# Performance work log

Hardware: AMD Instinct MI355X
Metric: run time of the kernel (lower is better)

The kernel has to match this reference:

```python
import jax, jax.numpy as jnp
import numpy as np

K, N, NE, NI, MA, IN, B = 8, 512, 256, 256, 3, 128, 1024
H, UNFOLDS = 0.04, 6
DT = H / UNFOLDS
STATE = NE * MA + NI * MA + NE + NI + N  # 2560


def inv_softplus(x):
    return float(np.log(np.expm1(x)))


def piecewise_sigmoid(x, S_a=0.9, S_c=0.0):
    a = S_a / 2.0
    c = S_c
    k = 0.5 / (1.0 - 2.0 * a)  # = 5.0 for S_a=0.9
    x1, x2, x3, x4 = c + a - 1.0, c - a, c + a, c + 1.0 - a
    quad_rise = k * (x - x1) * (x - x1)
    linear = x - c + 0.5
    quad_cap = 1.0 - k * (x - x4) * (x - x4)
    out = jnp.where(x < x1, 0.0, quad_rise)
    out = jnp.where(x >= x2, linear, out)
    out = jnp.where(x > x3, quad_cap, out)
    out = jnp.where(x > x4, 1.0, out)
    return out


def setup_inputs():
    key = jax.random.key(0)
    ks = jax.random.split(key, 6)
    m = (jax.random.uniform(ks[0], (K, N, N)) > 0.5).astype(jnp.float32)  # sparsity masks
    W_raw = jax.random.normal(ks[1], (K, N, N)) * np.float32(np.sqrt(2.0 / N)) * m
    W_in = jax.random.normal(ks[2], (K, N, IN)) * 0.1
    lo, hi = inv_softplus(0.25), inv_softplus(10.0)
    taus = jnp.asarray([lo + (hi - lo) * ai / (MA - 1) for ai in range(MA)], dtype=jnp.float32)
    log_tau_a = jnp.tile(taus[None, None, :], (K, NE, 1))
    return {
        "inputs": jax.random.normal(ks[3], (B, IN), dtype=jnp.float32),
        "state": jax.random.uniform(ks[4], (K, B, STATE), dtype=jnp.float32),
        "W_raw": W_raw,
        "sparsity_masks": m,
        "W_in": W_in,
        "a_0": jnp.full((K, N), 0.35, jnp.float32),
        "log_tau_d": jnp.full((K, N), inv_softplus(0.1), jnp.float32),
        "log_tau_a_E": log_tau_a,
        "log_c_E": jnp.full((K, NE, MA), -3.0, jnp.float32),
        "c_0_E": jnp.zeros((K, NE, MA), jnp.float32),
        "log_tau_a_I": log_tau_a,
        "log_c_I": jnp.full((K, NI, MA), -3.0, jnp.float32),
        "c_0_I": jnp.zeros((K, NI, MA), jnp.float32),
        "log_tau_b_rec_E": jnp.full((K, NE), inv_softplus(1.0), jnp.float32),
        "log_tau_b_rel_E": jnp.full((K, NE), inv_softplus(0.25), jnp.float32),
        "log_tau_b_rec_I": jnp.full((K, NI), inv_softplus(1.0), jnp.float32),
        "log_tau_b_rel_I": jnp.full((K, NI), inv_softplus(0.25), jnp.float32),
        "readout_ids": jnp.zeros((K,), dtype=jnp.int32),  # 0=synaptic,1=rate,2=dendritic
    }


def _forward(inputs, state, W_raw, sparsity_masks, W_in, a_0, log_tau_d,
             log_tau_a_E, log_c_E, c_0_E, log_tau_a_I, log_c_I, c_0_I,
             log_tau_b_rec_E, log_tau_b_rel_E, log_tau_b_rec_I, log_tau_b_rel_I,
             readout_ids):
    sp = jax.nn.softplus
    # unpack flat state (K,B,STATE)
    i0 = NE * MA; i1 = i0 + NI * MA; i2 = i1 + NE; i3 = i2 + NI
    aE = state[:, :, :i0].reshape(K, B, NE, MA)
    aI = state[:, :, i0:i1].reshape(K, B, NI, MA)
    bE = state[:, :, i1:i2]          # (K,B,NE)
    bI = state[:, :, i2:i3]          # (K,B,NI)
    x = state[:, :, i3:]             # (K,B,N)
    # Dale-constrained effective recurrent weights
    W_pos = sp(W_raw)
    W_eff = jnp.concatenate([W_pos[:, :, :NE], -W_pos[:, :, NE:]], axis=2) * sparsity_masks
    # time-constant gains
    gx = DT / sp(log_tau_d)[:, None]                    # (K,1,N)
    gaE = DT / sp(log_tau_a_E)[:, None]                 # (K,1,NE,MA)
    gaI = DT / sp(log_tau_a_I)[:, None]
    cE = sp(log_c_E)[:, None]                           # (K,1,NE,MA)
    cI = sp(log_c_I)[:, None]
    grecE = (DT / sp(log_tau_b_rec_E))[:, None]         # (K,1,NE)
    grelE = (DT / sp(log_tau_b_rel_E))[:, None]
    grecI = (DT / sp(log_tau_b_rec_I))[:, None]
    grelI = (DT / sp(log_tau_b_rel_I))[:, None]
    in_cur = jnp.einsum('kni,bi->kbn', W_in, inputs)    # constant across unfolds

    def rate_syn(aE, aI, bE, bI, x):
        thr = a_0[:, None] + jnp.concatenate(
            [jnp.sum(aE + c_0_E[:, None], axis=-1),
             jnp.sum(aI + c_0_I[:, None], axis=-1)], axis=-1)
        r = piecewise_sigmoid(x - thr)                  # (K,B,N)
        s = r * jnp.concatenate([bE, bI], axis=-1)      # depression-scaled output
        return r, s

    def step(carry, _):
        aE, aI, bE, bI, x = carry
        r, s = rate_syn(aE, aI, bE, bI, x)
        rE, rI = r[..., :NE], r[..., NE:]
        syn = jnp.einsum('knm,kbm->kbn', W_eff, s) + in_cur
        x = (x + gx * syn) / (1.0 + gx)                 # semi-implicit Euler
        aE = (aE + gaE * cE * rE[..., None]) / (1.0 + gaE)
        aI = (aI + gaI * cI * rI[..., None]) / (1.0 + gaI)
        bE = (bE + grecE) / (1.0 + grecE + grelE * rE)
        bI = (bI + grecI) / (1.0 + grecI + grelI * rI)
        return (aE, aI, bE, bI, x), None

    (aE, aI, bE, bI, x), _ = jax.lax.scan(step, (aE, aI, bE, bI, x), None, length=UNFOLDS)
    r, s = rate_syn(aE, aI, bE, bI, x)
    rid = readout_ids[:, None, None]
    out = jnp.where(rid == 0, s, jnp.where(rid == 1, r, x))
    new_state = jnp.concatenate(
        [aE.reshape(K, B, -1), aI.reshape(K, B, -1), bE, bI, x], axis=-1)
    return out, new_state


def reference(inputs, state, W_raw, sparsity_masks, W_in, a_0, log_tau_d,
              log_tau_a_E, log_c_E, c_0_E, log_tau_a_I, log_c_I, c_0_I,
              log_tau_b_rec_E, log_tau_b_rel_E, log_tau_b_rec_I, log_tau_b_rel_I,
              readout_ids):
    return _forward(inputs, state, W_raw, sparsity_masks, W_in, a_0, log_tau_d,
                    log_tau_a_E, log_c_E, c_0_E, log_tau_a_I, log_c_I, c_0_I,
                    log_tau_b_rec_E, log_tau_b_rel_E, log_tau_b_rec_I, log_tau_b_rel_I,
                    readout_ids)
```

## Files before the change

### kernel.cpp

```cpp
#include <hip/hip_runtime.h>
#include <stdint.h>

#define K_ 8
#define N_ 512
#define NE_ 256
#define MA_ 3
#define IN_ 128
#define B_ 1024
#define STATE_ 2560
#define UNFOLDS_ 6
#define DT_ (0.04f / 6.0f)

typedef __attribute__((ext_vector_type(8))) short short8;
typedef __attribute__((ext_vector_type(4))) float floatx4;

__device__ __forceinline__ float b2f(uint16_t u) {
    union { uint32_t i; float f; } v; v.i = ((uint32_t)u) << 16; return v.f;
}
__device__ __forceinline__ uint16_t f2b(float f) {
    union { float f; uint32_t i; } v; v.f = f;
    uint32_t i = v.i;
    uint32_t r = i + 0x7FFFu + ((i >> 16) & 1u);
    return (uint16_t)(r >> 16);
}
__device__ __forceinline__ uint32_t pack2(uint16_t lo, uint16_t hi) {
    return (uint32_t)lo | ((uint32_t)hi << 16);
}
__device__ __forceinline__ float loadf(const void* p, size_t i, int f32) {
    return f32 ? ((const float*)p)[i] : b2f(((const uint16_t*)p)[i]);
}
__device__ __forceinline__ float ntloadf(const void* p, size_t i, int f32) {
    return f32 ? __builtin_nontemporal_load((const float*)p + i)
               : b2f(__builtin_nontemporal_load((const uint16_t*)p + i));
}
__device__ __forceinline__ float spf(float x) {
    return (x > 20.f) ? x : log1pf(expf(x));
}
__device__ __forceinline__ float psig(float x) {
    float t1 = x + 0.55f;
    float q1 = 5.f * t1 * t1;
    float t2 = x - 0.55f;
    float q2 = 1.f - 5.f * t2 * t2;
    float out = (x < -0.55f) ? 0.f : q1;
    out = (x >= -0.45f) ? (x + 0.5f) : out;
    out = (x > 0.45f) ? q2 : out;
    out = (x > 0.55f) ? 1.f : out;
    return out;
}

__global__ void srnn_detect_kernel(const uint16_t* canary, int* flag) {
    __shared__ int cnt;
    if (threadIdx.x == 0) cnt = 0;
    __syncthreads();
    int bad = 0;
    for (int i = threadIdx.x; i < 4096; i += 256) {
        uint16_t u = canary[i];
        int e = (u >> 7) & 0xFF;
        if (e >= 0xC0) bad++;
    }
    atomicAdd(&cnt, bad);
    __syncthreads();
    if (threadIdx.x == 0) flag[0] = (cnt >= 16) ? 1 : 0;
}

__global__ void srnn_params_kernel(
    const void* a0, const void* ltd,
    const void* ltaE, const void* lcE, const void* c0E,
    const void* ltaI, const void* lcI, const void* c0I,
    const void* lbrecE, const void* lbrelE,
    const void* lbrecI, const void* lbrelI,
    const int* flag, float* P)
{
    const int f = flag[0];
    int idx = blockIdx.x * 256 + threadIdx.x;
    if (idx >= K_ * N_) return;
    int n = idx & (N_ - 1);
    int k = idx >> 9;
    float gx = DT_ / spf(loadf(ltd, idx, f));
    float thr0 = loadf(a0, idx, f);

    const void *lta, *lc, *c0, *lbrec, *lbrel;
    int nn;
    if (n < NE_) { nn = n;        lta = ltaE; lc = lcE; c0 = c0E; lbrec = lbrecE; lbrel = lbrelE; }
    else         { nn = n - NE_;  lta = ltaI; lc = lcI; c0 = c0I; lbrec = lbrecI; lbrel = lbrelI; }
    int base3 = (k * NE_ + nn) * MA_;
    int base1 = k * NE_ + nn;

    float amul[3], ainv[3];
    #pragma unroll
    for (int j = 0; j < 3; ++j) {
        float ga = DT_ / spf(loadf(lta, base3 + j, f));
        float c  = spf(loadf(lc, base3 + j, f));
        amul[j] = ga * c;
        ainv[j] = 1.f / (1.f + ga);
        thr0 += loadf(c0, base3 + j, f);
    }
    float grec = DT_ / spf(loadf(lbrec, base1, f));
    float grel = DT_ / spf(loadf(lbrel, base1, f));

    const int KN = K_ * N_;
    P[0*KN + idx] = gx;
    P[1*KN + idx] = 1.f / (1.f + gx);
    P[2*KN + idx] = thr0;
    P[3*KN + idx] = grec;
    P[4*KN + idx] = grel;
    P[5*KN + idx] = amul[0]; P[6*KN + idx] = amul[1]; P[7*KN + idx] = amul[2];
    P[8*KN + idx] = ainv[0]; P[9*KN + idx] = ainv[1]; P[10*KN + idx] = ainv[2];
}

__global__ __launch_bounds__(256) void srnn_wsw_kernel(
    const void* __restrict__ Wraw, const void* __restrict__ mask,
    const int* __restrict__ flag, uint16_t* __restrict__ Wsw)
{
    __shared__ float tile[16 * 516];
    const int f = flag[0];
    const int nt = blockIdx.x, k = blockIdx.y, t = threadIdx.x;
    const size_t base = (size_t)k * N_ * N_ + (size_t)nt * 16 * N_;
    #pragma unroll
    for (int i = 0; i < 32; ++i) {
        int idx = i * 256 + t;
        int row = idx >> 9, m = idx & 511;
        size_t gi = base + (size_t)row * N_ + m;
        float w = spf(ntloadf(Wraw, gi, f)) * ntloadf(mask, gi, f);
        if (m >= NE_) w = -w;
        tile[row * 516 + m] = w;
    }
    __syncthreads();
    uint16_t* outb = Wsw + ((size_t)k * 32 + nt) * (16 * 64 * 8);
    #pragma unroll
    for (int i = 0; i < 4; ++i) {
        int id = i * 256 + t;
        int ks = id >> 6, L = id & 63;
        int row = L & 15, quad = L >> 4;
        const float* src = &tile[row * 516 + ks * 32 + quad * 8];
        uint4 v;
        v.x = pack2(f2b(src[0]), f2b(src[1]));
        v.y = pack2(f2b(src[2]), f2b(src[3]));
        v.z = pack2(f2b(src[4]), f2b(src[5]));
        v.w = pack2(f2b(src[6]), f2b(src[7]));
        *(uint4*)(outb + (size_t)id * 8) = v;
    }
}

__global__ __launch_bounds__(256) void srnn_winsw_kernel(
    const void* __restrict__ Win, const int* __restrict__ flag,
    uint16_t* __restrict__ Winsw)
{
    __shared__ float tile[16 * 132];
    const int f = flag[0];
    const int nt = blockIdx.x, k = blockIdx.y, t = threadIdx.x;
    const size_t base = (size_t)k * N_ * IN_ + (size_t)nt * 16 * IN_;
    #pragma unroll
    for (int i = 0; i < 8; ++i) {
        int idx = i * 256 + t;
        int row = idx >> 7, c = idx & 127;
        tile[row * 132 + c] = ntloadf(Win, base + (size_t)row * IN_ + c, f);
    }
    __syncthreads();
    uint16_t* outb = Winsw + ((size_t)k * 32 + nt) * (4 * 64 * 8);
    {
        int id = t;
        int ks = id >> 6, L = id & 63;
        int row = L & 15, quad = L >> 4;
        const float* src = &tile[row * 132 + ks * 32 + quad * 8];
        uint4 v;
        v.x = pack2(f2b(src[0]), f2b(src[1]));
        v.y = pack2(f2b(src[2]), f2b(src[3]));
        v.z = pack2(f2b(src[4]), f2b(src[5]));
        v.w = pack2(f2b(src[6]), f2b(src[7]));
        *(uint4*)(outb + (size_t)id * 8) = v;
    }
}

__global__ __launch_bounds__(512, 1)
void srnn_main_kernel(const void* __restrict__ state,
                      const void* __restrict__ inputs,
                      const uint16_t* __restrict__ Wsw,
                      const uint16_t* __restrict__ Winsw,
                      const float* __restrict__ P,
                      const int* __restrict__ readout,
                      const int* __restrict__ flag,
                      void* __restrict__ out)
{
    __shared__ __align__(16) uint16_t sT[16 * 520];
    __shared__ __align__(16) float synT[16 * 516];

    const int f = flag[0];
    const int t = threadIdx.x;
    const int k = blockIdx.x & 7;
    const int b0 = (blockIdx.x >> 3) * 16;
    const int n = t;
    const int lane = t & 63, w = t >> 6;
    const int bq = lane & 15, quad = lane >> 4;

    const int KN = K_ * N_;
    const int pi = k * N_ + n;
    const float gx = P[0*KN+pi], ivgx = P[1*KN+pi], thr0 = P[2*KN+pi];
    const float grec = P[3*KN+pi], grel = P[4*KN+pi];
    const float amul0 = P[5*KN+pi], amul1 = P[6*KN+pi], amul2 = P[7*KN+pi];
    const float ainv0 = P[8*KN+pi], ainv1 = P[9*KN+pi], ainv2 = P[10*KN+pi];

    #pragma unroll
    for (int q = 0; q < 4; ++q) {
        int idx = q * 512 + t;
        int bb = idx >> 7, i = idx & 127;
        sT[bb * 520 + i] = f2b(ntloadf(inputs, (size_t)(b0 + bb) * IN_ + i, f));
    }

    float a0v[16], a1v[16], a2v[16], bv[16], xv[16], ic[16];
    #pragma unroll
    for (int bb = 0; bb < 16; ++bb) {
        size_t sb = ((size_t)k * B_ + b0 + bb) * STATE_;
        a0v[bb] = ntloadf(state, sb + 3 * n + 0, f);
        a1v[bb] = ntloadf(state, sb + 3 * n + 1, f);
        a2v[bb] = ntloadf(state, sb + 3 * n + 2, f);
        bv[bb]  = ntloadf(state, sb + 1536 + n, f);
        xv[bb]  = ntloadf(state, sb + 2048 + n, f);
    }
    __syncthreads();

    const uint16_t* bpe = sT + bq * 520 + quad * 8;

    {
        const uint16_t* api = Winsw + ((size_t)(k * 32 + 4 * w) * 4) * 512 + (size_t)lane * 8;
        floatx4 d0 = {0.f,0.f,0.f,0.f}, d1 = d0, d2 = d0, d3 = d0;
        #pragma unroll
        for (int ks = 0; ks < 4; ++ks) {
            short8 bf = *(const short8*)(bpe + ks * 32);
            short8 a0f = *(const short8*)(api + (0 * 4 + ks) * 512);
            short8 a1f = *(const short8*)(api + (1 * 4 + ks) * 512);
            short8 a2f = *(const short8*)(api + (2 * 4 + ks) * 512);
            short8 a3f = *(const short8*)(api + (3 * 4 + ks) * 512);
            d0 = __builtin_amdgcn_mfma_f32_16x16x32_bf16(a0f, bf, d0, 0, 0, 0);
            d1 = __builtin_amdgcn_mfma_f32_16x16x32_bf16(a1f, bf, d1, 0, 0, 0);
            d2 = __builtin_amdgcn_mfma_f32_16x16x32_bf16(a2f, bf, d2, 0, 0, 0);
            d3 = __builtin_amdgcn_mfma_f32_16x16x32_bf16(a3f, bf, d3, 0, 0, 0);
        }
        const int nb = w * 64 + quad * 4;
        *(floatx4*)(&synT[bq * 516 + nb +  0]) = d0;
        *(floatx4*)(&synT[bq * 516 + nb + 16]) = d1;
        *(floatx4*)(&synT[bq * 516 + nb + 32]) = d2;
        *(floatx4*)(&synT[bq * 516 + nb + 48]) = d3;
    }
    __syncthreads();
    #pragma unroll
    for (int bb = 0; bb < 16; ++bb) ic[bb] = synT[bb * 516 + n];
    __syncthreads();

    const uint16_t* ape = Wsw + (size_t)k * 32 * 8192 + (size_t)(4 * w) * 8192 + (size_t)lane * 8;

    for (int step = 0; step < UNFOLDS_; ++step) {
        #pragma unroll
        for (int bb = 0; bb < 16; ++bb) {
            float thr = thr0 + a0v[bb] + a1v[bb] + a2v[bb];
            float r = psig(xv[bb] - thr);
            float s = r * bv[bb];
            a0v[bb] = fmaf(amul0, r, a0v[bb]) * ainv0;
            a1v[bb] = fmaf(amul1, r, a1v[bb]) * ainv1;
            a2v[bb] = fmaf(amul2, r, a2v[bb]) * ainv2;
            bv[bb] = (bv[bb] + grec) / (1.f + grec + grel * r);
            sT[bb * 520 + n] = f2b(s);
        }
        __syncthreads();

        floatx4 c0 = {0.f, 0.f, 0.f, 0.f}, c1 = c0, c2 = c0, c3 = c0;
        #pragma unroll 4
        for (int ks = 0; ks < 16; ++ks) {
            short8 bf = *(const short8*)(bpe + ks * 32);
            short8 af0 = *(const short8*)(ape + ks * 512);
            short8 af1 = *(const short8*)(ape + 8192 + ks * 512);
            short8 af2 = *(const short8*)(ape + 16384 + ks * 512);
            short8 af3 = *(const short8*)(ape + 24576 + ks * 512);
            c0 = __builtin_amdgcn_mfma_f32_16x16x32_bf16(af0, bf, c0, 0, 0, 0);
            c1 = __builtin_amdgcn_mfma_f32_16x16x32_bf16(af1, bf, c1, 0, 0, 0);
            c2 = __builtin_amdgcn_mfma_f32_16x16x32_bf16(af2, bf, c2, 0, 0, 0);
            c3 = __builtin_amdgcn_mfma_f32_16x16x32_bf16(af3, bf, c3, 0, 0, 0);
        }
        {
            const int nb = w * 64 + quad * 4;
            *(floatx4*)(&synT[bq * 516 + nb +  0]) = c0;
            *(floatx4*)(&synT[bq * 516 + nb + 16]) = c1;
            *(floatx4*)(&synT[bq * 516 + nb + 32]) = c2;
            *(floatx4*)(&synT[bq * 516 + nb + 48]) = c3;
        }
        __syncthreads();

        #pragma unroll
        for (int bb = 0; bb < 16; ++bb) {
            float syn = synT[bb * 516 + n] + ic[bb];
            xv[bb] = fmaf(gx, syn, xv[bb]) * ivgx;
        }
    }

    const int rid = readout[k];
    if (f) {
        float* outp = (float*)out;
        float* nst = outp + (size_t)K_ * B_ * N_;
        #pragma unroll
        for (int bb = 0; bb < 16; ++bb) {
            float thr = thr0 + a0v[bb] + a1v[bb] + a2v[bb];
            float r = psig(xv[bb] - thr);
            float s = r * bv[bb];
            float o = (rid == 0) ? s : ((rid == 1) ? r : xv[bb]);
            size_t ob = (size_t)k * B_ + b0 + bb;
            __builtin_nontemporal_store(o, outp + ob * N_ + n);
            float* st = nst + ob * STATE_;
            __builtin_nontemporal_store(a0v[bb], st + 3 * n + 0);
            __builtin_nontemporal_store(a1v[bb], st + 3 * n + 1);
            __builtin_nontemporal_store(a2v[bb], st + 3 * n + 2);
            __builtin_nontemporal_store(bv[bb], st + 1536 + n);
            __builtin_nontemporal_store(xv[bb], st + 2048 + n);
        }
    } else {
        uint16_t* outp = (uint16_t*)out;
        uint16_t* nst = outp + (size_t)K_ * B_ * N_;
        #pragma unroll
        for (int bb = 0; bb < 16; ++bb) {
            float thr = thr0 + a0v[bb] + a1v[bb] + a2v[bb];
            float r = psig(xv[bb] - thr);
            float s = r * bv[bb];
            float o = (rid == 0) ? s : ((rid == 1) ? r : xv[bb]);
            size_t ob = (size_t)k * B_ + b0 + bb;
            __builtin_nontemporal_store(f2b(o), outp + ob * N_ + n);
            uint16_t* st = nst + ob * STATE_;
            __builtin_nontemporal_store(f2b(a0v[bb]), st + 3 * n + 0);
            __builtin_nontemporal_store(f2b(a1v[bb]), st + 3 * n + 1);
            __builtin_nontemporal_store(f2b(a2v[bb]), st + 3 * n + 2);
            __builtin_nontemporal_store(f2b(bv[bb]), st + 1536 + n);
            __builtin_nontemporal_store(f2b(xv[bb]), st + 2048 + n);
        }
    }
}

extern "C" void kernel_launch(void* const* d_in, const int* in_sizes, int n_in,
                              void* d_out, int out_size, void* d_ws, size_t ws_size,
                              hipStream_t stream) {
    const void* inputs = d_in[0];
    const void* state  = d_in[1];
    const void* Wraw   = d_in[2];
    const void* mask   = d_in[3];
    const void* Win    = d_in[4];
    const void* a0     = d_in[5];
    const void* ltd    = d_in[6];
    const void* ltaE   = d_in[7];
    const void* lcE    = d_in[8];
    const void* c0E    = d_in[9];
    const void* ltaI   = d_in[10];
    const void* lcI    = d_in[11];
    const void* c0I    = d_in[12];
    const void* lbrecE = d_in[13];
    const void* lbrelE = d_in[14];
    const void* lbrecI = d_in[15];
    const void* lbrelI = d_in[16];
    const int* readout = (const int*)d_in[17];

    char* ws = (char*)d_ws;
    int* flag       = (int*)ws;
    float* P        = (float*)(ws + 256);
    uint16_t* Wsw   = (uint16_t*)(ws + 256 + 180224);
    uint16_t* Winsw = (uint16_t*)(ws + 256 + 180224 + 4194304);

    srnn_detect_kernel<<<dim3(1), dim3(256), 0, stream>>>((const uint16_t*)Wraw, flag);
    srnn_params_kernel<<<dim3(16), dim3(256), 0, stream>>>(
        a0, ltd, ltaE, lcE, c0E, ltaI, lcI, c0I, lbrecE, lbrelE, lbrecI, lbrelI, flag, P);
    srnn_wsw_kernel<<<dim3(32, 8), dim3(256), 0, stream>>>(Wraw, mask, flag, Wsw);
    srnn_winsw_kernel<<<dim3(32, 8), dim3(256), 0, stream>>>(Win, flag, Winsw);
    srnn_main_kernel<<<dim3(512), dim3(512), 0, stream>>>(
        state, inputs, Wsw, Winsw, P, readout, flag, d_out);
}
```

Measured before the change: 343.7 us.

## Process 32 batch rows per block, reusing weight fragments across two batch tiles

The main kernel now runs 1024 threads per block covering two 16-row batch sub-tiles, so each loaded W fragment feeds two MFMAs and global weight traffic per batch row is halved. The input projection is folded into every step's MFMA accumulation instead of being precomputed once and held in registers. The x update moves to the start of the next step, and the final x update moves into the epilogue. Per-neuron parameters are staged in shared memory, and the b-update divide is replaced by a fast reciprocal using a precomputed 1+grec. This trades fewer blocks (256), larger shared-memory use and redundant input-projection MFMAs for better weight reuse.

After: 392.5 us. 14.2% more time.

```diff
diff --git a/kernel.cpp b/kernel.cpp
--- a/kernel.cpp
+++ b/kernel.cpp
@@ -106,6 +106,7 @@
     P[4*KN + idx] = grel;
     P[5*KN + idx] = amul[0]; P[6*KN + idx] = amul[1]; P[7*KN + idx] = amul[2];
     P[8*KN + idx] = ainv[0]; P[9*KN + idx] = ainv[1]; P[10*KN + idx] = ainv[2];
+    P[11*KN + idx] = 1.f + grec;
 }
 
 __global__ __launch_bounds__(256) void srnn_wsw_kernel(
@@ -172,7 +173,7 @@
     }
 }
 
-__global__ __launch_bounds__(512, 1)
+__global__ __launch_bounds__(1024, 4)
 void srnn_main_kernel(const void* __restrict__ state,
                       const void* __restrict__ inputs,
                       const uint16_t* __restrict__ Wsw,
@@ -182,35 +183,40 @@
                       const int* __restrict__ flag,
                       void* __restrict__ out)
 {
-    __shared__ __align__(16) uint16_t sT[16 * 520];
-    __shared__ __align__(16) float synT[16 * 516];
+    __shared__ __align__(16) uint16_t sT[2][16 * 520];
+    __shared__ __align__(16) float synT[2][16 * 516];
+    __shared__ __align__(16) uint16_t U[2][16 * 136];
+    __shared__ float Pl[12 * 512];
 
     const int f = flag[0];
     const int t = threadIdx.x;
     const int k = blockIdx.x & 7;
-    const int b0 = (blockIdx.x >> 3) * 16;
-    const int n = t;
+    const int b0 = (blockIdx.x >> 3) * 32;
+    const int sub = t >> 9;
+    const int n = t & 511;
     const int lane = t & 63, w = t >> 6;
     const int bq = lane & 15, quad = lane >> 4;
 
-    const int KN = K_ * N_;
-    const int pi = k * N_ + n;
-    const float gx = P[0*KN+pi], ivgx = P[1*KN+pi], thr0 = P[2*KN+pi];
-    const float grec = P[3*KN+pi], grel = P[4*KN+pi];
-    const float amul0 = P[5*KN+pi], amul1 = P[6*KN+pi], amul2 = P[7*KN+pi];
-    const float ainv0 = P[8*KN+pi], ainv1 = P[9*KN+pi], ainv2 = P[10*KN+pi];
-
+    {
+        const int KN = K_ * N_;
+        #pragma unroll
+        for (int q = 0; q < 6; ++q) {
+            int idx = q * 1024 + t;
+            Pl[idx] = P[(idx >> 9) * KN + k * N_ + (idx & 511)];
+        }
+    }
     #pragma unroll
     for (int q = 0; q < 4; ++q) {
-        int idx = q * 512 + t;
-        int bb = idx >> 7, i = idx & 127;
-        sT[bb * 520 + i] = f2b(ntloadf(inputs, (size_t)(b0 + bb) * IN_ + i, f));
-    }
-
-    float a0v[16], a1v[16], a2v[16], bv[16], xv[16], ic[16];
+        int idx = q * 1024 + t;
+        int ss = idx >> 11, rem = idx & 2047;
+        int bb = rem >> 7, ii = rem & 127;
+        U[ss][bb * 136 + ii] =
+            f2b(ntloadf(inputs, (size_t)(b0 + ss * 16 + bb) * IN_ + ii, f));
+    }
+    float a0v[16], a1v[16], a2v[16], bv[16], xv[16];
     #pragma unroll
     for (int bb = 0; bb < 16; ++bb) {
-        size_t sb = ((size_t)k * B_ + b0 + bb) * STATE_;
+        size_t sb = ((size_t)k * B_ + b0 + sub * 16 + bb) * STATE_;
         a0v[bb] = ntloadf(state, sb + 3 * n + 0, f);
         a1v[bb] = ntloadf(state, sb + 3 * n + 1, f);
         a2v[bb] = ntloadf(state, sb + 3 * n + 2, f);
@@ -219,115 +225,114 @@
     }
     __syncthreads();
 
-    const uint16_t* bpe = sT + bq * 520 + quad * 8;
-
-    {
-        const uint16_t* api = Winsw + ((size_t)(k * 32 + 4 * w) * 4) * 512 + (size_t)lane * 8;
-        floatx4 d0 = {0.f,0.f,0.f,0.f}, d1 = d0, d2 = d0, d3 = d0;
-        #pragma unroll
-        for (int ks = 0; ks < 4; ++ks) {
-            short8 bf = *(const short8*)(bpe + ks * 32);
-            short8 a0f = *(const short8*)(api + (0 * 4 + ks) * 512);
-            short8 a1f = *(const short8*)(api + (1 * 4 + ks) * 512);
-            short8 a2f = *(const short8*)(api + (2 * 4 + ks) * 512);
-            short8 a3f = *(const short8*)(api + (3 * 4 + ks) * 512);
-            d0 = __builtin_amdgcn_mfma_f32_16x16x32_bf16(a0f, bf, d0, 0, 0, 0);
-            d1 = __builtin_amdgcn_mfma_f32_16x16x32_bf16(a1f, bf, d1, 0, 0, 0);
-            d2 = __builtin_amdgcn_mfma_f32_16x16x32_bf16(a2f, bf, d2, 0, 0, 0);
-            d3 = __builtin_amdgcn_mfma_f32_16x16x32_bf16(a3f, bf, d3, 0, 0, 0);
-        }
-        const int nb = w * 64 + quad * 4;
-        *(floatx4*)(&synT[bq * 516 + nb +  0]) = d0;
-        *(floatx4*)(&synT[bq * 516 + nb + 16]) = d1;
-        *(floatx4*)(&synT[bq * 516 + nb + 32]) = d2;
-        *(floatx4*)(&synT[bq * 516 + nb + 48]) = d3;
-    }
-    __syncthreads();
-    #pragma unroll
-    for (int bb = 0; bb < 16; ++bb) ic[bb] = synT[bb * 516 + n];
-    __syncthreads();
-
-    const uint16_t* ape = Wsw + (size_t)k * 32 * 8192 + (size_t)(4 * w) * 8192 + (size_t)lane * 8;
+    const uint16_t* bpe0 = sT[0] + bq * 520 + quad * 8;
+    const uint16_t* bpe1 = sT[1] + bq * 520 + quad * 8;
+    const uint16_t* upe0 = U[0] + bq * 136 + quad * 8;
+    const uint16_t* upe1 = U[1] + bq * 136 + quad * 8;
+    const uint16_t* ape  = Wsw + (size_t)k * 262144 + (size_t)(2 * w) * 8192
+                               + (size_t)lane * 8;
+    const uint16_t* apie = Winsw + (size_t)(k * 32 + 2 * w) * 2048
+                                 + (size_t)lane * 8;
 
     for (int step = 0; step < UNFOLDS_; ++step) {
-        #pragma unroll
-        for (int bb = 0; bb < 16; ++bb) {
-            float thr = thr0 + a0v[bb] + a1v[bb] + a2v[bb];
-            float r = psig(xv[bb] - thr);
-            float s = r * bv[bb];
-            a0v[bb] = fmaf(amul0, r, a0v[bb]) * ainv0;
-            a1v[bb] = fmaf(amul1, r, a1v[bb]) * ainv1;
-            a2v[bb] = fmaf(amul2, r, a2v[bb]) * ainv2;
-            bv[bb] = (bv[bb] + grec) / (1.f + grec + grel * r);
-            sT[bb * 520 + n] = f2b(s);
+        {
+            const float gx = Pl[0*512+n], ivgx = Pl[1*512+n];
+            if (step) {
+                #pragma unroll
+                for (int bb = 0; bb < 16; ++bb)
+                    xv[bb] = fmaf(gx, synT[sub][bb * 516 + n], xv[bb]) * ivgx;
+            }
+            const float thr0 = Pl[2*512+n], grec = Pl[3*512+n], grel = Pl[4*512+n];
+            const float am0 = Pl[5*512+n], am1 = Pl[6*512+n], am2 = Pl[7*512+n];
+            const float ai0 = Pl[8*512+n], ai1 = Pl[9*512+n], ai2 = Pl[10*512+n];
+            const float ogr = Pl[11*512+n];
+            #pragma unroll
+            for (int bb = 0; bb < 16; ++bb) {
+                float thr = thr0 + a0v[bb] + a1v[bb] + a2v[bb];
+                float r = psig(xv[bb] - thr);
+                float s = r * bv[bb];
+                a0v[bb] = fmaf(am0, r, a0v[bb]) * ai0;
+                a1v[bb] = fmaf(am1, r, a1v[bb]) * ai1;
+                a2v[bb] = fmaf(am2, r, a2v[bb]) * ai2;
+                bv[bb] = (bv[bb] + grec) *
+                         __builtin_amdgcn_rcpf(fmaf(grel, r, ogr));
+                sT[sub][bb * 520 + n] = f2b(s);
+            }
         }
         __syncthreads();
 
-        floatx4 c0 = {0.f, 0.f, 0.f, 0.f}, c1 = c0, c2 = c0, c3 = c0;
-        #pragma unroll 4
-        for (int ks = 0; ks < 16; ++ks) {
-            short8 bf = *(const short8*)(bpe + ks * 32);
-            short8 af0 = *(const short8*)(ape + ks * 512);
-            short8 af1 = *(const short8*)(ape + 8192 + ks * 512);
-            short8 af2 = *(const short8*)(ape + 16384 + ks * 512);
-            short8 af3 = *(const short8*)(ape + 24576 + ks * 512);
-            c0 = __builtin_amdgcn_mfma_f32_16x16x32_bf16(af0, bf, c0, 0, 0, 0);
-            c1 = __builtin_amdgcn_mfma_f32_16x16x32_bf16(af1, bf, c1, 0, 0, 0);
-            c2 = __builtin_amdgcn_mfma_f32_16x16x32_bf16(af2, bf, c2, 0, 0, 0);
-            c3 = __builtin_amdgcn_mfma_f32_16x16x32_bf16(af3, bf, c3, 0, 0, 0);
-        }
         {
-            const int nb = w * 64 + quad * 4;
-            *(floatx4*)(&synT[bq * 516 + nb +  0]) = c0;
-            *(floatx4*)(&synT[bq * 516 + nb + 16]) = c1;
-            *(floatx4*)(&synT[bq * 516 + nb + 32]) = c2;
-            *(floatx4*)(&synT[bq * 516 + nb + 48]) = c3;
+            floatx4 c00 = {0.f,0.f,0.f,0.f}, c01 = c00, c10 = c00, c11 = c00;
+            #pragma unroll 2
+            for (int ks = 0; ks < 16; ++ks) {
+                short8 bf0 = *(const short8*)(bpe0 + ks * 32);
+                short8 bf1 = *(const short8*)(bpe1 + ks * 32);
+                short8 af0 = *(const short8*)(ape + ks * 512);
+                short8 af1 = *(const short8*)(ape + 8192 + ks * 512);
+                c00 = __builtin_amdgcn_mfma_f32_16x16x32_bf16(af0, bf0, c00, 0, 0, 0);
+                c01 = __builtin_amdgcn_mfma_f32_16x16x32_bf16(af0, bf1, c01, 0, 0, 0);
+                c10 = __builtin_amdgcn_mfma_f32_16x16x32_bf16(af1, bf0, c10, 0, 0, 0);
+                c11 = __builtin_amdgcn_mfma_f32_16x16x32_bf16(af1, bf1, c11, 0, 0, 0);
+            }
+            #pragma unroll
+            for (int e = 0; e < 4; ++e) {
+                short8 bu0 = *(const short8*)(upe0 + e * 32);
+                short8 bu1 = *(const short8*)(upe1 + e * 32);
+                short8 aw0 = *(const short8*)(apie + e * 512);
+                short8 aw1 = *(const short8*)(apie + 2048 + e * 512);
+                c00 = __builtin_amdgcn_mfma_f32_16x16x32_bf16(aw0, bu0, c00, 0, 0, 0);
+                c01 = __builtin_amdgcn_mfma_f32_16x16x32_bf16(aw0, bu1, c01, 0, 0, 0);
+                c10 = __builtin_amdgcn_mfma_f32_16x16x32_bf16(aw1, bu0, c10, 0, 0, 0);
+                c11 = __builtin_amdgcn_mfma_f32_16x16x32_bf16(aw1, bu1, c11, 0, 0, 0);
+            }
+            const int nb = w * 32 + quad * 4;
+            *(floatx4*)(&synT[0][bq * 516 + nb +  0]) = c00;
+            *(floatx4*)(&synT[0][bq * 516 + nb + 16]) = c10;
+            *(floatx4*)(&synT[1][bq * 516 + nb +  0]) = c01;
+            *(floatx4*)(&synT[1][bq * 516 + nb + 16]) = c11;
         }
         __syncthreads();
-
-        #pragma unroll
-        for (int bb = 0; bb < 16; ++bb) {
-            float syn = synT[bb * 516 + n] + ic[bb];
-            xv[bb] = fmaf(gx, syn, xv[bb]) * ivgx;
-        }
     }
 
     const int rid = readout[k];
+    const float gx = Pl[0*512+n], ivgx = Pl[1*512+n], thr0 = Pl[2*512+n];
     if (f) {
         float* outp = (float*)out;
         float* nst = outp + (size_t)K_ * B_ * N_;
         #pragma unroll
         for (int bb = 0; bb < 16; ++bb) {
+            float x = fmaf(gx, synT[sub][bb * 516 + n], xv[bb]) * ivgx;
             float thr = thr0 + a0v[bb] + a1v[bb] + a2v[bb];
-            float r = psig(xv[bb] - thr);
+            float r = psig(x - thr);
             float s = r * bv[bb];
-            float o = (rid == 0) ? s : ((rid == 1) ? r : xv[bb]);
-            size_t ob = (size_t)k * B_ + b0 + bb;
+            float o = (rid == 0) ? s : ((rid == 1) ? r : x);
+            size_t ob = (size_t)k * B_ + b0 + sub * 16 + bb;
             __builtin_nontemporal_store(o, outp + ob * N_ + n);
             float* st = nst + ob * STATE_;
             __builtin_nontemporal_store(a0v[bb], st + 3 * n + 0);
             __builtin_nontemporal_store(a1v[bb], st + 3 * n + 1);
             __builtin_nontemporal_store(a2v[bb], st + 3 * n + 2);
             __builtin_nontemporal_store(bv[bb], st + 1536 + n);
-            __builtin_nontemporal_store(xv[bb], st + 2048 + n);
+            __builtin_nontemporal_store(x, st + 2048 + n);
         }
     } else {
         uint16_t* outp = (uint16_t*)out;
         uint16_t* nst = outp + (size_t)K_ * B_ * N_;
         #pragma unroll
         for (int bb = 0; bb < 16; ++bb) {
+            float x = fmaf(gx, synT[sub][bb * 516 + n], xv[bb]) * ivgx;
             float thr = thr0 + a0v[bb] + a1v[bb] + a2v[bb];
-            float r = psig(xv[bb] - thr);
+            float r = psig(x - thr);
             float s = r * bv[bb];
-            float o = (rid == 0) ? s : ((rid == 1) ? r : xv[bb]);
-            size_t ob = (size_t)k * B_ + b0 + bb;
+            float o = (rid == 0) ? s : ((rid == 1) ? r : x);
+            size_t ob = (size_t)k * B_ + b0 + sub * 16 + bb;
             __builtin_nontemporal_store(f2b(o), outp + ob * N_ + n);
             uint16_t* st = nst + ob * STATE_;
             __builtin_nontemporal_store(f2b(a0v[bb]), st + 3 * n + 0);
             __builtin_nontemporal_store(f2b(a1v[bb]), st + 3 * n + 1);
             __builtin_nontemporal_store(f2b(a2v[bb]), st + 3 * n + 2);
             __builtin_nontemporal_store(f2b(bv[bb]), st + 1536 + n);
-            __builtin_nontemporal_store(f2b(xv[bb]), st + 2048 + n);
+            __builtin_nontemporal_store(f2b(x), st + 2048 + n);
         }
     }
 }
@@ -357,14 +362,14 @@
     char* ws = (char*)d_ws;
     int* flag       = (int*)ws;
     float* P        = (float*)(ws + 256);
-    uint16_t* Wsw   = (uint16_t*)(ws + 256 + 180224);
-    uint16_t* Winsw = (uint16_t*)(ws + 256 + 180224 + 4194304);
+    uint16_t* Wsw   = (uint16_t*)(ws + 256 + 196608);
+    uint16_t* Winsw = (uint16_t*)(ws + 256 + 196608 + 4194304);
 
     srnn_detect_kernel<<<dim3(1), dim3(256), 0, stream>>>((const uint16_t*)Wraw, flag);
     srnn_params_kernel<<<dim3(16), dim3(256), 0, stream>>>(
         a0, ltd, ltaE, lcE, c0E, ltaI, lcI, c0I, lbrecE, lbrelE, lbrecI, lbrelI, flag, P);
     srnn_wsw_kernel<<<dim3(32, 8), dim3(256), 0, stream>>>(Wraw, mask, flag, Wsw);
     srnn_winsw_kernel<<<dim3(32, 8), dim3(256), 0, stream>>>(Win, flag, Winsw);
-    srnn_main_kernel<<<dim3(512), dim3(512), 0, stream>>>(
+    srnn_main_kernel<<<dim3(256), dim3(1024), 0, stream>>>(
         state, inputs, Wsw, Winsw, P, readout, flag, d_out);
 }
```
